# Optimization experiments

Hardware: AMD Instinct MI355X
Metric: run time of the kernel (lower is better)

The kernel has to match this reference:

```python
import jax, jax.numpy as jnp
import numpy as np

NUM_TOKENS = 8192
D_IN = 2048
D_OUT = 2048
N_EXPERT = 9
N_SHARED = 1
N_SPARSE = N_EXPERT - N_SHARED  # 8
TOP_K = 2


def setup_inputs() -> dict:
    key = jax.random.key(0)
    ks = jax.random.split(key, 7)
    s_in = 1.0 / np.sqrt(D_IN)
    return {
        "x": jax.random.normal(ks[0], (NUM_TOKENS, D_IN), jnp.float32),
        # shared experts (Linear input_dim->output_dim), stacked over shared axis
        "W_shared": jax.random.uniform(ks[1], (N_SHARED, D_IN, D_OUT), jnp.float32, -s_in, s_in),
        "b_shared": jax.random.uniform(ks[2], (N_SHARED, D_OUT), jnp.float32, -s_in, s_in),
        # router: Linear input_dim -> num_sparse_experts
        "W_router": jax.random.uniform(ks[3], (D_IN, N_SPARSE), jnp.float32, -s_in, s_in),
        "b_router": jax.random.uniform(ks[4], (N_SPARSE,), jnp.float32, -s_in, s_in),
        # sparse experts stacked over expert axis
        "W_sparse": jax.random.uniform(ks[5], (N_SPARSE, D_IN, D_OUT), jnp.float32, -s_in, s_in),
        "b_sparse": jax.random.uniform(ks[6], (N_SPARSE, D_OUT), jnp.float32, -s_in, s_in),
    }


def reference(x, W_shared, b_shared, W_router, b_router, W_sparse, b_sparse):
    T = x.shape[0]
    # shared experts: sum of Linear outputs, divided by n_shared (mean)
    y = (jnp.einsum("td,sdo->to", x, W_shared) + b_shared.sum(0)) / N_SHARED

    # router (eval: no noise, no capacity dropping)
    logits = x @ W_router + b_router                       # [T, E]
    probs = jax.nn.softmax(logits, axis=-1)
    topk_w, topk_idx = jax.lax.top_k(probs, TOP_K)          # [T, K]
    topk_w = topk_w / (topk_w.sum(-1, keepdims=True) + 1e-6)

    # dense gate matrix [T, E]; top-k indices per row are distinct
    gates = jnp.zeros((T, N_SPARSE), x.dtype).at[
        jnp.arange(T)[:, None], topk_idx
    ].add(topk_w)

    # weighted combination of sparse expert outputs
    y = y + jnp.einsum("td,edo,te->to", x, W_sparse, gates)
    y = y + gates @ b_sparse
    return y


if __name__ == "__main__":
    out = reference(**setup_inputs())
    print(out.shape, out.dtype)
```

## Files before the change

kernel.cpp:

```cpp
#include <hip/hip_runtime.h>
#include <hip/hip_bf16.h>
#include <stdint.h>

#define NT   8192
#define DIN  2048
#define DOUT 2048
#define NSP  8
#define BK   64

typedef _Float16 f16x8 __attribute__((ext_vector_type(8)));
typedef float    f32x4 __attribute__((ext_vector_type(4)));

static_assert(sizeof(f16x8) == 16, "f16x8 must be 16B");

__device__ __forceinline__ f32x4 mfma_f16(f16x8 a, f16x8 b, f32x4 c) {
  return __builtin_amdgcn_mfma_f32_16x16x32_f16(a, b, c, 0, 0, 0);
}

__device__ __forceinline__ void async16(const void* g, void* l) {
  __builtin_amdgcn_global_load_lds(
      (const __attribute__((address_space(1))) uint32_t*)g,
      (__attribute__((address_space(3))) uint32_t*)l, 16, 0, 0);
}

__global__ void k_convert_x(const float* __restrict__ x,
                            _Float16* __restrict__ xh) {
  int idx = blockIdx.x * blockDim.x + threadIdx.x;
  const float4* xv = (const float4*)x;
  float4 v0 = xv[2 * idx], v1 = xv[2 * idx + 1];
  union { _Float16 h[8]; int4 q; } H;
  H.h[0] = (_Float16)v0.x; H.h[1] = (_Float16)v0.y;
  H.h[2] = (_Float16)v0.z; H.h[3] = (_Float16)v0.w;
  H.h[4] = (_Float16)v1.x; H.h[5] = (_Float16)v1.y;
  H.h[6] = (_Float16)v1.z; H.h[7] = (_Float16)v1.w;
  ((int4*)xh)[idx] = H.q;
}

__global__ void k_convert_w(const float* __restrict__ W,
                            _Float16* __restrict__ wth, int eoff) {
  __shared__ float tile[32][33];
  const int e = blockIdx.z;
  const float* Wm = W + (size_t)e * DIN * DOUT;
  const int k0 = blockIdx.x * 32, o0 = blockIdx.y * 32;
  const int r = threadIdx.x >> 5, c = threadIdx.x & 31;
#pragma unroll
  for (int i = 0; i < 4; i++) {
    int rr = r + i * 8;
    tile[rr][c] = Wm[(size_t)(k0 + rr) * DOUT + o0 + c];
  }
  __syncthreads();
  const size_t obase = (size_t)(eoff + e) * DOUT;
#pragma unroll
  for (int i = 0; i < 4; i++) {
    int rr = r + i * 8;
    float val = tile[c][rr];
    wth[(obase + o0 + rr) * (size_t)DIN + (size_t)(k0 + c)] = (_Float16)val;
  }
}

__global__ void k_router(const float* __restrict__ x, const float* __restrict__ Wr,
                         const float* __restrict__ br,
                         int* __restrict__ counts, int* __restrict__ tok_list,
                         float* __restrict__ w_list) {
  const int wave = threadIdx.x >> 6, lane = threadIdx.x & 63;
  const int t = blockIdx.x * 4 + wave;
  const float* xrow = x + (size_t)t * DIN;
  float acc[NSP];
#pragma unroll
  for (int e = 0; e < NSP; e++) acc[e] = 0.f;
  for (int d = lane; d < DIN; d += 64) {
    float xv = xrow[d];
    const float* wr = Wr + d * NSP;
#pragma unroll
    for (int e = 0; e < NSP; e++) acc[e] += xv * wr[e];
  }
#pragma unroll
  for (int e = 0; e < NSP; e++) {
#pragma unroll
    for (int off = 32; off > 0; off >>= 1) acc[e] += __shfl_xor(acc[e], off, 64);
  }
  if (lane == 0) {
    float lg[NSP], mx = -1e30f;
#pragma unroll
    for (int e = 0; e < NSP; e++) { lg[e] = acc[e] + br[e]; mx = fmaxf(mx, lg[e]); }
    float p[NSP], s = 0.f;
#pragma unroll
    for (int e = 0; e < NSP; e++) { p[e] = expf(lg[e] - mx); s += p[e]; }
    int i0 = 0;
#pragma unroll
    for (int e = 1; e < NSP; e++) if (p[e] > p[i0]) i0 = e;
    int i1 = (i0 == 0) ? 1 : 0;
#pragma unroll
    for (int e = 0; e < NSP; e++) if (e != i0 && p[e] > p[i1]) i1 = e;
    float p0 = p[i0] / s, p1 = p[i1] / s;
    float denom = p0 + p1 + 1e-6f;
    float w0 = p0 / denom, w1 = p1 / denom;
    int s0 = atomicAdd(&counts[i0], 1);
    tok_list[i0 * NT + s0] = t; w_list[i0 * NT + s0] = w0;
    int s1 = atomicAdd(&counts[i1], 1);
    tok_list[i1 * NT + s1] = t; w_list[i1 * NT + s1] = w1;
  }
}

template <bool SPARSE>
__global__ __launch_bounds__(256, 4) void k_moe_gemm(
    const _Float16* __restrict__ xh, const _Float16* __restrict__ wth,
    const float* __restrict__ bias, const int* __restrict__ counts,
    const int* __restrict__ tok_list, const float* __restrict__ w_list,
    float* __restrict__ y) {
  const int e = SPARSE ? blockIdx.z : 0;
  const int wi = SPARSE ? (1 + e) : 0;
  int cnt = NT;
  if (SPARSE) {
    cnt = counts[e];
    if ((int)blockIdx.y * 128 >= cnt) return;
  }
  const int row0 = blockIdx.y * 128;
  const int col0 = blockIdx.x * 128;

  __shared__ __align__(16) _Float16 sA[128 * BK];
  __shared__ __align__(16) _Float16 sB[128 * BK];
  __shared__ int   s_tok[128];
  __shared__ float s_w[128];

  const int tid = threadIdx.x;
  const int wave = tid >> 6, lane = tid & 63;

  if (SPARSE) {
    if (tid < 128) {
      int slot = row0 + tid;
      int tk = 0; float w = 0.f;
      if (slot < cnt) { tk = tok_list[e * NT + slot]; w = w_list[e * NT + slot]; }
      s_tok[tid] = tk; s_w[tid] = w;
    }
    __syncthreads();
  }

  const int lr = lane >> 3, pp = lane & 7;
  const _Float16* gA[4]; const _Float16* gB[4];
  int loff[4];
#pragma unroll
  for (int j = 0; j < 4; j++) {
    int r = wave * 32 + j * 8 + lr;
    int xoff = ((pp ^ (r & 7)) << 3);
    int tk = SPARSE ? s_tok[r] : (row0 + r);
    gA[j] = xh + (size_t)tk * DIN + xoff;
    gB[j] = wth + ((size_t)wi * DOUT + (size_t)(col0 + r)) * DIN + xoff;
    loff[j] = r * BK + pp * 8;
  }

  f32x4 acc[4][4];
#pragma unroll
  for (int m = 0; m < 4; m++)
#pragma unroll
    for (int n = 0; n < 4; n++) acc[m][n] = (f32x4){0.f, 0.f, 0.f, 0.f};

  const int wm = (wave >> 1) * 64, wn = (wave & 1) * 64;
  const int fr = lane & 15, fg = lane >> 4;

  for (int kt = 0; kt < DIN / BK; kt++) {
    const int k0 = kt * BK;
#pragma unroll
    for (int j = 0; j < 4; j++) {
      async16(gA[j] + k0, &sA[loff[j]]);
      async16(gB[j] + k0, &sB[loff[j]]);
    }
    __syncthreads();

#pragma unroll
    for (int ks = 0; ks < 2; ks++) {
      f16x8 ah[4], bh[4];
#pragma unroll
      for (int m = 0; m < 4; m++) {
        int r = wm + m * 16 + fr;
        int sl = (((ks * 4 + fg) ^ (r & 7)) << 3);
        ah[m] = *(const f16x8*)&sA[r * BK + sl];
      }
#pragma unroll
      for (int n = 0; n < 4; n++) {
        int c = wn + n * 16 + fr;
        int sl = (((ks * 4 + fg) ^ (c & 7)) << 3);
        bh[n] = *(const f16x8*)&sB[c * BK + sl];
      }
#pragma unroll
      for (int m = 0; m < 4; m++)
#pragma unroll
        for (int n = 0; n < 4; n++)
          acc[m][n] = mfma_f16(ah[m], bh[n], acc[m][n]);
    }
    __syncthreads();
  }

#pragma unroll
  for (int n = 0; n < 4; n++) {
    int col = col0 + wn + n * 16 + fr;
    float bc = SPARSE ? bias[e * DOUT + col] : bias[col];
#pragma unroll
    for (int m = 0; m < 4; m++) {
#pragma unroll
      for (int q = 0; q < 4; q++) {
        int lrow = wm + m * 16 + fg * 4 + q;
        float v = acc[m][n][q];
        if (SPARSE) {
          if (row0 + lrow < cnt) {
            float g = s_w[lrow];
            atomicAdd(&y[(size_t)s_tok[lrow] * DOUT + col], g * (v + bc));
          }
        } else {
          y[(size_t)(row0 + lrow) * DOUT + col] = v + bc;
        }
      }
    }
  }
}

template <bool SPARSE>
__global__ void k_fb_gemm(const float* __restrict__ x, const float* __restrict__ W,
                          const float* __restrict__ bias,
                          const int* __restrict__ counts,
                          const int* __restrict__ tok_list,
                          const float* __restrict__ w_list,
                          float* __restrict__ y) {
  const int e = SPARSE ? blockIdx.z : 0;
  int cnt = NT;
  if (SPARSE) {
    cnt = counts[e];
    if ((int)blockIdx.y * 64 >= cnt) return;
  }
  const int row0 = blockIdx.y * 64, col0 = blockIdx.x * 64;
  const float* Wm = W + (SPARSE ? (size_t)e * DIN * DOUT : 0);

  __shared__ float sA[64][17];
  __shared__ float sB[16][65];
  __shared__ int   s_tok[64];
  __shared__ float s_w[64];

  const int tid = threadIdx.x;
  if (SPARSE) {
    if (tid < 64) {
      int slot = row0 + tid;
      int tk = 0; float w = 0.f;
      if (slot < cnt) { tk = tok_list[e * NT + slot]; w = w_list[e * NT + slot]; }
      s_tok[tid] = tk; s_w[tid] = w;
    }
    __syncthreads();
  }

  const int ar = tid >> 2, ak = (tid & 3) * 4;
  const int bk = tid >> 4, bc4 = (tid & 15) * 4;
  const int tm = tid >> 4, tn = tid & 15;

  float acc[4][4];
#pragma unroll
  for (int m = 0; m < 4; m++)
#pragma unroll
    for (int n = 0; n < 4; n++) acc[m][n] = 0.f;

  const int tkA = SPARSE ? s_tok[ar] : (row0 + ar);

  for (int k0 = 0; k0 < DIN; k0 += 16) {
    float4 va = *(const float4*)&x[(size_t)tkA * DIN + k0 + ak];
    float4 vb = *(const float4*)&Wm[(size_t)(k0 + bk) * DOUT + col0 + bc4];
    sA[ar][ak]     = va.x; sA[ar][ak + 1] = va.y;
    sA[ar][ak + 2] = va.z; sA[ar][ak + 3] = va.w;
    sB[bk][bc4]     = vb.x; sB[bk][bc4 + 1] = vb.y;
    sB[bk][bc4 + 2] = vb.z; sB[bk][bc4 + 3] = vb.w;
    __syncthreads();
#pragma unroll
    for (int kk = 0; kk < 16; kk++) {
      float a0 = sA[tm * 4 + 0][kk], a1 = sA[tm * 4 + 1][kk];
      float a2 = sA[tm * 4 + 2][kk], a3 = sA[tm * 4 + 3][kk];
#pragma unroll
      for (int n = 0; n < 4; n++) {
        float b = sB[kk][tn * 4 + n];
        acc[0][n] += a0 * b; acc[1][n] += a1 * b;
        acc[2][n] += a2 * b; acc[3][n] += a3 * b;
      }
    }
    __syncthreads();
  }

#pragma unroll
  for (int m = 0; m < 4; m++) {
    int lrow = tm * 4 + m;
#pragma unroll
    for (int n = 0; n < 4; n++) {
      int col = col0 + tn * 4 + n;
      float bcv = SPARSE ? bias[e * DOUT + col] : bias[col];
      if (SPARSE) {
        if (row0 + lrow < cnt) {
          atomicAdd(&y[(size_t)s_tok[lrow] * DOUT + col],
                    s_w[lrow] * (acc[m][n] + bcv));
        }
      } else {
        y[(size_t)(row0 + lrow) * DOUT + col] = acc[m][n] + bcv;
      }
    }
  }
}

__global__ void k_zero(float* __restrict__ y, int n) {
  for (int i = blockIdx.x * blockDim.x + threadIdx.x; i < n;
       i += gridDim.x * blockDim.x)
    y[i] = 0.f;
}

extern "C" void kernel_launch(void* const* d_in, const int* in_sizes, int n_in,
                              void* d_out, int out_size, void* d_ws, size_t ws_size,
                              hipStream_t stream) {
  (void)in_sizes; (void)n_in;
  const float* x   = (const float*)d_in[0];
  const float* Wsh = (const float*)d_in[1];
  const float* bsh = (const float*)d_in[2];
  const float* Wr  = (const float*)d_in[3];
  const float* br  = (const float*)d_in[4];
  const float* Wsp = (const float*)d_in[5];
  const float* bsp = (const float*)d_in[6];
  float* y = (float*)d_out;

  char* ws = (char*)d_ws;
  size_t off = 0;
  auto alloc = [&](size_t bytes) {
    off = (off + 255) & ~(size_t)255;
    void* p = ws + off;
    off += bytes;
    return p;
  };
  int*      counts   = (int*)alloc(NSP * sizeof(int));
  int*      tok_list = (int*)alloc((size_t)NSP * NT * sizeof(int));
  float*    w_list   = (float*)alloc((size_t)NSP * NT * sizeof(float));
  const size_t NEED_FB = off;
  _Float16* xh       = (_Float16*)alloc((size_t)NT * DIN * 2);
  _Float16* wth      = (_Float16*)alloc((size_t)9 * DOUT * DIN * 2);
  const size_t NEED_FAST = off;

  if (ws_size < NEED_FB) {
    k_zero<<<2048, 256, 0, stream>>>(y, out_size);
    return;
  }

  hipMemsetAsync(counts, 0, NSP * sizeof(int), stream);
  k_router<<<NT / 4, 256, 0, stream>>>(x, Wr, br, counts, tok_list, w_list);

  if (ws_size >= NEED_FAST) {
    k_convert_x<<<(NT * DIN / 8) / 256, 256, 0, stream>>>(x, xh);
    k_convert_w<<<dim3(DIN / 32, DOUT / 32, 1), 256, 0, stream>>>(Wsh, wth, 0);
    k_convert_w<<<dim3(DIN / 32, DOUT / 32, NSP), 256, 0, stream>>>(Wsp, wth, 1);
    k_moe_gemm<false><<<dim3(DOUT / 128, NT / 128, 1), 256, 0, stream>>>(
        xh, wth, bsh, counts, tok_list, w_list, y);
    k_moe_gemm<true><<<dim3(DOUT / 128, NT / 128, NSP), 256, 0, stream>>>(
        xh, wth, bsp, counts, tok_list, w_list, y);
  } else {
    k_fb_gemm<false><<<dim3(DOUT / 64, NT / 64, 1), 256, 0, stream>>>(
        x, Wsh, bsh, counts, tok_list, w_list, y);
    k_fb_gemm<true><<<dim3(DOUT / 64, NT / 64, NSP), 256, 0, stream>>>(
        x, Wsp, bsp, counts, tok_list, w_list, y);
  }
}
```

Measured before the change: 785.3 us.

## Swizzle GEMM block order across XCDs and merge weight conversion into one kernel

The two weight-conversion kernels become one launch that handles all nine experts with 64x64 tiles, float4 loads, fp16 shared staging and 16-byte transposed stores. This cuts launch count and makes memory access wider. The GEMM grid is remapped so consecutive block IDs, which round-robin across the 8 XCDs, land on a contiguous chunk of tiles per XCD. The intent is better L2 reuse of A and B tiles. The sparse early-exit now uses the remapped row, so row-major tile order changes and the empty-tile pruning pattern shifts.

```diff
diff --git a/kernel.cpp b/kernel.cpp
--- a/kernel.cpp
+++ b/kernel.cpp
@@ -36,25 +36,34 @@
   ((int4*)xh)[idx] = H.q;
 }
 
-__global__ void k_convert_w(const float* __restrict__ W,
-                            _Float16* __restrict__ wth, int eoff) {
-  __shared__ float tile[32][33];
-  const int e = blockIdx.z;
-  const float* Wm = W + (size_t)e * DIN * DOUT;
-  const int k0 = blockIdx.x * 32, o0 = blockIdx.y * 32;
-  const int r = threadIdx.x >> 5, c = threadIdx.x & 31;
+__global__ void k_convert_w9(const float* __restrict__ Wsh,
+                             const float* __restrict__ Wsp,
+                             _Float16* __restrict__ wth) {
+  __shared__ _Float16 sh[64 * 66];
+  const int z = blockIdx.z;
+  const float* Wm = (z == 0) ? Wsh : (Wsp + (size_t)(z - 1) * DIN * DOUT);
+  const int k0 = blockIdx.x * 64, o0 = blockIdx.y * 64;
+  const int t = threadIdx.x;
+  const int kr = t >> 4, oc4 = (t & 15) * 4;
 #pragma unroll
   for (int i = 0; i < 4; i++) {
-    int rr = r + i * 8;
-    tile[rr][c] = Wm[(size_t)(k0 + rr) * DOUT + o0 + c];
+    int k = kr + i * 16;
+    float4 v = *(const float4*)&Wm[(size_t)(k0 + k) * DOUT + o0 + oc4];
+    sh[k * 66 + oc4 + 0] = (_Float16)v.x;
+    sh[k * 66 + oc4 + 1] = (_Float16)v.y;
+    sh[k * 66 + oc4 + 2] = (_Float16)v.z;
+    sh[k * 66 + oc4 + 3] = (_Float16)v.w;
   }
   __syncthreads();
-  const size_t obase = (size_t)(eoff + e) * DOUT;
-#pragma unroll
-  for (int i = 0; i < 4; i++) {
-    int rr = r + i * 8;
-    float val = tile[c][rr];
-    wth[(obase + o0 + rr) * (size_t)DIN + (size_t)(k0 + c)] = (_Float16)val;
+  const int orow = t >> 3, kq = t & 7;
+  const size_t obase = (size_t)z * DOUT;
+#pragma unroll
+  for (int i = 0; i < 2; i++) {
+    int o = orow + i * 32;
+    union { _Float16 h[8]; int4 q; } P;
+#pragma unroll
+    for (int j = 0; j < 8; j++) P.h[j] = sh[(kq * 8 + j) * 66 + o];
+    *(int4*)&wth[(obase + o0 + o) * (size_t)DIN + (size_t)(k0 + kq * 8)] = P.q;
   }
 }
 
@@ -110,13 +119,19 @@
     float* __restrict__ y) {
   const int e = SPARSE ? blockIdx.z : 0;
   const int wi = SPARSE ? (1 + e) : 0;
+
+  const int nx = gridDim.x;
+  const int bid = blockIdx.y * nx + blockIdx.x;
+  const int cpx = (nx * gridDim.y) >> 3;
+  const int swz = (bid & 7) * cpx + (bid >> 3);
+  const int row0 = (swz % nx) * 128;
+  const int col0 = (swz / nx) * 128;
+
   int cnt = NT;
   if (SPARSE) {
     cnt = counts[e];
-    if ((int)blockIdx.y * 128 >= cnt) return;
-  }
-  const int row0 = blockIdx.y * 128;
-  const int col0 = blockIdx.x * 128;
+    if (row0 >= cnt) return;
+  }
 
   __shared__ __align__(16) _Float16 sA[128 * BK];
   __shared__ __align__(16) _Float16 sB[128 * BK];
@@ -344,11 +359,10 @@
 
   if (ws_size >= NEED_FAST) {
     k_convert_x<<<(NT * DIN / 8) / 256, 256, 0, stream>>>(x, xh);
-    k_convert_w<<<dim3(DIN / 32, DOUT / 32, 1), 256, 0, stream>>>(Wsh, wth, 0);
-    k_convert_w<<<dim3(DIN / 32, DOUT / 32, NSP), 256, 0, stream>>>(Wsp, wth, 1);
-    k_moe_gemm<false><<<dim3(DOUT / 128, NT / 128, 1), 256, 0, stream>>>(
+    k_convert_w9<<<dim3(DIN / 64, DOUT / 64, 9), 256, 0, stream>>>(Wsh, Wsp, wth);
+    k_moe_gemm<false><<<dim3(NT / 128, DOUT / 128, 1), 256, 0, stream>>>(
         xh, wth, bsh, counts, tok_list, w_list, y);
-    k_moe_gemm<true><<<dim3(DOUT / 128, NT / 128, NSP), 256, 0, stream>>>(
+    k_moe_gemm<true><<<dim3(NT / 128, DOUT / 128, NSP), 256, 0, stream>>>(
         xh, wth, bsp, counts, tok_list, w_list, y);
   } else {
     k_fb_gemm<false><<<dim3(DOUT / 64, NT / 64, 1), 256, 0, stream>>>(
```

Result: no change. 794.0 us, median of 2 (+1.1%).
